# Performance work log

Measured on AMD Instinct MI355X. Metric: run time of the kernel, lower is better.

The kernel has to match this reference:

```python
import jax, jax.numpy as jnp
import numpy as np

D = 512
MOMENTUM = 0.99
NEG_INF = -1.0e9


def setup_inputs() -> dict:
    key = jax.random.key(0)
    ks = jax.random.split(key, 16)
    B, Lq, Lk = 16, 1024, 1024
    s = 0.02
    inp = {
        "uncond_q": jax.random.normal(ks[0], (B, D), jnp.float32),
        "q": jax.random.normal(ks[1], (B, Lq, D), jnp.float32),
        "k": jax.random.normal(ks[2], (B, Lk, D), jnp.float32),
        "v": jax.random.normal(ks[3], (B, Lk, D), jnp.float32),
        "src_key_padding_mask": jax.random.randint(ks[4], (B, Lk), 0, 2) > 0,
        "fallback_score": jnp.zeros((1,), jnp.float32),
        # parameters (torch Linear: y = x @ W.T + b)
        "Wv": jax.random.normal(ks[5], (D, D), jnp.float32) * s,
        "bv": jnp.zeros((D,), jnp.float32),
        "Wf": jax.random.normal(ks[6], (D, D), jnp.float32) * s,
        "bf": jnp.zeros((D,), jnp.float32),
        "W1": jax.random.normal(ks[7], (D, D), jnp.float32) * s,
        "b1": jnp.zeros((D,), jnp.float32),
        "W2": jax.random.normal(ks[8], (D // 2, D), jnp.float32) * s,
        "b2": jnp.zeros((D // 2,), jnp.float32),
        "W3": jax.random.normal(ks[9], (1, D // 2), jnp.float32) * s,
        "b3": jnp.zeros((1,), jnp.float32),
    }
    return inp


def _scorer(x, W1, b1, W2, b2, W3, b3):
    h = jax.nn.relu(x @ W1.T + b1)
    h = jax.nn.relu(h @ W2.T + b2)
    return jnp.tanh(h @ W3.T + b3)


def reference(uncond_q, q, k, v, src_key_padding_mask, fallback_score,
              Wv, bv, Wf, bf, W1, b1, W2, b2, W3, b3):
    B, Lq, _ = q.shape
    v_p = v @ Wv.T + bv                                  # [B,Lk,D]
    default_values = (uncond_q @ Wf.T + bf)[:, None, :]  # [B,1,D]

    scores = jnp.einsum('bqd,bkd->bqk', q, k) / jnp.sqrt(jnp.float32(D))

    # EMA fallback-score update (training mode), detached from grads
    bmax = jax.lax.stop_gradient(scores.max())
    bmin = jax.lax.stop_gradient(scores.min())
    fb = MOMENTUM * fallback_score[0] + (1.0 - MOMENTUM) * (bmax + bmin) / 2.0

    scores = jnp.where(src_key_padding_mask[:, None, :], NEG_INF, scores)
    fb_col = jnp.broadcast_to(fb, (B, Lq, 1))
    scores = jnp.concatenate([scores, fb_col], axis=-1)   # [B,Lq,Lk+1]
    weights = jax.nn.softmax(scores, axis=-1)

    v_padded = jnp.concatenate([v_p, default_values], axis=1)  # [B,Lk+1,D]
    out = jnp.einsum('bqk,bkd->bqd', weights, v_padded)

    return (_scorer(out, W1, b1, W2, b2, W3, b3),
            _scorer(default_values, W1, b1, W2, b2, W3, b3))
```

## Files before the change

### kernel.cpp

```cpp
#include <hip/hip_runtime.h>

typedef _Float16 f16;
typedef f16  f16x8 __attribute__((ext_vector_type(8)));
typedef f16  f16x4 __attribute__((ext_vector_type(4)));
typedef __fp16 fp16x2 __attribute__((ext_vector_type(2)));
typedef float f32x4 __attribute__((ext_vector_type(4)));

__device__ __forceinline__ void gld_lds16(const f16* g, void* l) {
  __builtin_amdgcn_global_load_lds((const __attribute__((address_space(1))) void*)g,
                                   (__attribute__((address_space(3))) void*)l,
                                   16, 0, 0);
}

__device__ __forceinline__ f16x8 pack8(float4 a, float4 b) {
  union { f16x8 v; fp16x2 h[4]; } u;
  u.h[0] = __builtin_amdgcn_cvt_pkrtz(a.x, a.y);
  u.h[1] = __builtin_amdgcn_cvt_pkrtz(a.z, a.w);
  u.h[2] = __builtin_amdgcn_cvt_pkrtz(b.x, b.y);
  u.h[3] = __builtin_amdgcn_cvt_pkrtz(b.z, b.w);
  return u.v;
}

enum { EPI_SCORES = 0, EPI_RELU = 2, EPI_OUT = 3, EPI_BIASR = 4 };

template<int EPI, bool XMAP>
__global__ __launch_bounds__(256)
void gemm_bt(const f16* __restrict__ A, const f16* __restrict__ B, void* __restrict__ C,
             int lda, int ldb, int ldc, int K,
             long long sA, long long sB, long long sC,
             const float* __restrict__ bias, float scale,
             const float* __restrict__ wfb, const float* __restrict__ dvv,
             int nx, int nbz)
{
  __shared__ __align__(16) f16 As[4][128][32];
  __shared__ __align__(16) f16 Bs[4][128][32];
  const int tid  = threadIdx.x;
  const int lane = tid & 63;
  const int w    = tid >> 6;
  const int wm   = w >> 1, wn = w & 1;

  const int lin = blockIdx.x;
  int bz, bj;
  if constexpr (XMAP) {
    const int xcd = lin & 7, rest = lin >> 3;
    const int grp = rest / nbz;
    bj = rest - grp * nbz;
    bz = xcd + (grp << 3);
  } else {
    bz = lin / nbz; bj = lin - bz * nbz;
  }
  const int m0 = (bj / nx) * 128, n0 = (bj % nx) * 128;
  const f16* Ab = A + (size_t)bz * sA + (size_t)m0 * lda;
  const f16* Bb = B + (size_t)bz * sB + (size_t)n0 * ldb;

  f32x4 acc[4][4] = {};
  const int nsteps = K >> 5;

#define STAGE(bufb, ks)                                                              \
  {                                                                                  \
    const int k0_ = (ks) << 5;                                                       \
    _Pragma("unroll")                                                                \
    for (int i = 0; i < 2; ++i) {                                                    \
      const int ci = i * 256 + tid;                                                  \
      const int r  = ci >> 2;                                                        \
      const int sg = (ci & 3) ^ ((r >> 1) & 3);                                      \
      gld_lds16(Ab + (size_t)r * lda + k0_ + sg * 8,                                 \
                (char*)As + (bufb) + (size_t)(i * 256 + w * 64) * 16);               \
      gld_lds16(Bb + (size_t)r * ldb + k0_ + sg * 8,                                 \
                (char*)Bs + (bufb) + (size_t)(i * 256 + w * 64) * 16);               \
    }                                                                                \
  }

  STAGE(0, 0)
  if (1 < nsteps) STAGE(8192, 1)
  if (2 < nsteps) STAGE(16384, 2)

  const int elemoff = (((lane >> 4) ^ ((lane >> 1) & 3)) << 3);

  int cur = 0;
  for (int t = 0; t < nsteps; ++t) {
    if (t + 2 < nsteps)      asm volatile("s_waitcnt vmcnt(8)" ::: "memory");
    else if (t + 1 < nsteps) asm volatile("s_waitcnt vmcnt(4)" ::: "memory");
    else                     asm volatile("s_waitcnt vmcnt(0)" ::: "memory");
    __builtin_amdgcn_s_barrier();
    __builtin_amdgcn_sched_barrier(0);
    if (t + 3 < nsteps) STAGE(((cur + 3) & 3) * 8192, t + 3)
    f16x8 af[4], bfr[4];
#pragma unroll
    for (int m = 0; m < 4; ++m)
      af[m] = *(const f16x8*)&As[cur][wm * 64 + m * 16 + (lane & 15)][elemoff];
#pragma unroll
    for (int n = 0; n < 4; ++n)
      bfr[n] = *(const f16x8*)&Bs[cur][wn * 64 + n * 16 + (lane & 15)][elemoff];
    __builtin_amdgcn_s_setprio(1);
#pragma unroll
    for (int m = 0; m < 4; ++m)
#pragma unroll
      for (int n = 0; n < 4; ++n)
        acc[m][n] = __builtin_amdgcn_mfma_f32_16x16x32_f16(af[m], bfr[n], acc[m][n], 0, 0, 0);
    __builtin_amdgcn_s_setprio(0);
    cur = (cur + 1) & 3;
  }
#undef STAGE

  const int col_l = lane & 15;
  const int row_l = (lane >> 4) << 2;

  {
    f16* Ch = (f16*)C + (size_t)bz * sC + (size_t)m0 * ldc + n0;
#pragma unroll
    for (int m = 0; m < 4; ++m)
#pragma unroll
      for (int n = 0; n < 4; ++n)
#pragma unroll
        for (int r = 0; r < 4; ++r) {
          const int rr = wm * 64 + m * 16 + row_l + r;
          const int cc = wn * 64 + n * 16 + col_l;
          float val = acc[m][n][r];
          if constexpr (EPI == EPI_RELU) { val += bias[n0 + cc]; val = fmaxf(val, 0.0f); }
          if constexpr (EPI == EPI_BIASR) val += bias[m0 + rr];
          if constexpr (EPI == EPI_OUT)
            val += wfb[bz * 1024 + m0 + rr] * dvv[bz * 512 + n0 + cc];
          Ch[(size_t)rr * ldc + cc] = (f16)val;
        }
  }
  (void)scale;
}

__global__ __launch_bounds__(512, 2)
void gemm256_scores(const float* __restrict__ A, const float* __restrict__ B, f16* __restrict__ C,
                    float scale, float* __restrict__ mmarr)
{
  __shared__ __align__(16) f16 As[3][256][32];
  __shared__ __align__(16) f16 Bs[3][256][32];
  __shared__ float redm[8], redn[8];
  const int tid  = threadIdx.x;
  const int lane = tid & 63;
  const int w    = tid >> 6;
  const int wm   = w >> 2, wn = w & 3;
  const int lin  = blockIdx.x;
  const int xcd = lin & 7, rest = lin >> 3;
  const int bj  = rest & 15;
  const int bz  = xcd + ((rest >> 4) << 3);
  const int m0 = (bj >> 2) * 256, n0 = (bj & 3) * 256;
  const float* Ab = A + (size_t)bz * 524288 + (size_t)m0 * 512;
  const float* Bb = B + (size_t)bz * 524288 + (size_t)n0 * 512;

  const int r0  = tid >> 2;
  const int sg0 = (tid & 3) ^ ((r0 >> 1) & 3);
  const size_t offG = (size_t)r0 * 512 + sg0 * 8;
  f16* const dstA0 = (f16*)As + (size_t)tid * 8;
  f16* const dstB0 = (f16*)Bs + (size_t)tid * 8;

  f32x4 acc[8][4] = {};

#pragma unroll
  for (int s = 0; s < 2; ++s) {
    const int k0 = s << 5;
    float4 a0 = *(const float4*)(Ab + offG + k0);
    float4 a1 = *(const float4*)(Ab + offG + k0 + 4);
    float4 a2 = *(const float4*)(Ab + offG + k0 + 65536);
    float4 a3 = *(const float4*)(Ab + offG + k0 + 65540);
    float4 b0 = *(const float4*)(Bb + offG + k0);
    float4 b1 = *(const float4*)(Bb + offG + k0 + 4);
    float4 b2 = *(const float4*)(Bb + offG + k0 + 65536);
    float4 b3 = *(const float4*)(Bb + offG + k0 + 65540);
    *(f16x8*)(dstA0 + s * 8192)        = pack8(a0, a1);
    *(f16x8*)(dstA0 + s * 8192 + 4096) = pack8(a2, a3);
    *(f16x8*)(dstB0 + s * 8192)        = pack8(b0, b1);
    *(f16x8*)(dstB0 + s * 8192 + 4096) = pack8(b2, b3);
  }
  __syncthreads();

  const int fr = lane & 15;
  const int elemoff = (((lane >> 4) ^ ((lane >> 1) & 3)) << 3);

  int cur = 0;
  for (int t = 0; t < 16; ++t) {
    float4 a0, a1, a2, a3, b0, b1, b2, b3;
    if (t + 2 < 16) {
      const int k0 = (t + 2) << 5;
      a0 = *(const float4*)(Ab + offG + k0);
      a1 = *(const float4*)(Ab + offG + k0 + 4);
      a2 = *(const float4*)(Ab + offG + k0 + 65536);
      a3 = *(const float4*)(Ab + offG + k0 + 65540);
      b0 = *(const float4*)(Bb + offG + k0);
      b1 = *(const float4*)(Bb + offG + k0 + 4);
      b2 = *(const float4*)(Bb + offG + k0 + 65536);
      b3 = *(const float4*)(Bb + offG + k0 + 65540);
    }
    f16x8 af[8], bfr[4];
#pragma unroll
    for (int m = 0; m < 8; ++m)
      af[m] = *(const f16x8*)&As[cur][wm * 128 + m * 16 + fr][elemoff];
#pragma unroll
    for (int n = 0; n < 4; ++n)
      bfr[n] = *(const f16x8*)&Bs[cur][wn * 64 + n * 16 + fr][elemoff];
    __builtin_amdgcn_s_setprio(1);
#pragma unroll
    for (int m = 0; m < 8; ++m)
#pragma unroll
      for (int n = 0; n < 4; ++n)
        acc[m][n] = __builtin_amdgcn_mfma_f32_16x16x32_f16(af[m], bfr[n], acc[m][n], 0, 0, 0);
    __builtin_amdgcn_s_setprio(0);
    if (t + 2 < 16) {
      int wb = cur + 2; if (wb >= 3) wb -= 3;
      *(f16x8*)(dstA0 + wb * 8192)        = pack8(a0, a1);
      *(f16x8*)(dstA0 + wb * 8192 + 4096) = pack8(a2, a3);
      *(f16x8*)(dstB0 + wb * 8192)        = pack8(b0, b1);
      *(f16x8*)(dstB0 + wb * 8192 + 4096) = pack8(b2, b3);
    }
    __syncthreads();
    cur = (cur + 1 == 3) ? 0 : cur + 1;
  }

  const int col_l = lane & 15;
  const int row_l = (lane >> 4) << 2;
  f16* Ch = C + (size_t)bz * 1048576 + (size_t)m0 * 1024 + n0;
  float lmax = -3.402823466e38f, lmin = 3.402823466e38f;
#pragma unroll
  for (int m = 0; m < 8; ++m)
#pragma unroll
    for (int n = 0; n < 4; ++n)
#pragma unroll
      for (int r = 0; r < 4; ++r) {
        float val = acc[m][n][r] * scale;
        lmax = fmaxf(lmax, val); lmin = fminf(lmin, val);
        Ch[(size_t)(wm * 128 + m * 16 + row_l + r) * 1024 + (wn * 64 + n * 16 + col_l)] = (f16)val;
      }
#pragma unroll
  for (int off = 32; off >= 1; off >>= 1) {
    lmax = fmaxf(lmax, __shfl_xor(lmax, off));
    lmin = fminf(lmin, __shfl_xor(lmin, off));
  }
  if (lane == 0) { redm[w] = lmax; redn[w] = lmin; }
  __syncthreads();
  if (tid == 0) {
    float gm = redm[0], gn = redn[0];
#pragma unroll
    for (int i = 1; i < 8; ++i) { gm = fmaxf(gm, redm[i]); gn = fminf(gn, redn[i]); }
    mmarr[lin] = gm; mmarr[256 + lin] = gn;
  }
}

__global__ __launch_bounds__(256)
void gemm_vpt(const f16* __restrict__ A, const float* __restrict__ B, f16* __restrict__ C,
              const float* __restrict__ bias)
{
  __shared__ __align__(16) f16 As[3][128][32];
  __shared__ __align__(16) f16 Bs[3][128][32];
  const int tid  = threadIdx.x;
  const int lane = tid & 63;
  const int w    = tid >> 6;
  const int wm   = w >> 1, wn = w & 1;
  const int lin  = blockIdx.x;
  const int xcd = lin & 7, rest = lin >> 3;
  const int grp = rest >> 5, bj = rest & 31;
  const int bz  = xcd + (grp << 3);
  const int m0 = (bj >> 3) * 128, n0 = (bj & 7) * 128;
  const f16*   Ab = A + (size_t)m0 * 512;
  const float* Bb = B + (size_t)bz * 524288 + (size_t)n0 * 512;

  const int r0  = tid >> 2;
  const int sg0 = (tid & 3) ^ ((r0 >> 1) & 3);
  const size_t offA = (size_t)r0 * 512 + sg0 * 8;
  const size_t offB = (size_t)r0 * 512 + sg0 * 8;
  f16* const dstA0 = (f16*)As + (size_t)tid * 8;
  f16* const dstB0 = (f16*)Bs + (size_t)tid * 8;

  f32x4 acc[4][4] = {};

#pragma unroll
  for (int s = 0; s < 2; ++s) {
    const int k0 = s << 5;
    f16x8  a0 = *(const f16x8*)(Ab + offA + k0);
    f16x8  a1 = *(const f16x8*)(Ab + offA + k0 + 32768);
    float4 b0 = *(const float4*)(Bb + offB + k0);
    float4 b1 = *(const float4*)(Bb + offB + k0 + 4);
    float4 b2 = *(const float4*)(Bb + offB + k0 + 32768);
    float4 b3 = *(const float4*)(Bb + offB + k0 + 32772);
    *(f16x8*)(dstA0 + s * 4096)        = a0;
    *(f16x8*)(dstA0 + s * 4096 + 2048) = a1;
    *(f16x8*)(dstB0 + s * 4096)        = pack8(b0, b1);
    *(f16x8*)(dstB0 + s * 4096 + 2048) = pack8(b2, b3);
  }
  __syncthreads();

  const int fr = lane & 15;
  const int elemoff = (((lane >> 4) ^ ((lane >> 1) & 3)) << 3);

  int cur = 0;
  for (int t = 0; t < 16; ++t) {
    f16x8  a0, a1; float4 b0, b1, b2, b3;
    if (t + 2 < 16) {
      const int k0 = (t + 2) << 5;
      a0 = *(const f16x8*)(Ab + offA + k0);
      a1 = *(const f16x8*)(Ab + offA + k0 + 32768);
      b0 = *(const float4*)(Bb + offB + k0);
      b1 = *(const float4*)(Bb + offB + k0 + 4);
      b2 = *(const float4*)(Bb + offB + k0 + 32768);
      b3 = *(const float4*)(Bb + offB + k0 + 32772);
    }
    f16x8 af[4], bfr[4];
#pragma unroll
    for (int m = 0; m < 4; ++m)
      af[m] = *(const f16x8*)&As[cur][wm * 64 + m * 16 + fr][elemoff];
#pragma unroll
    for (int n = 0; n < 4; ++n)
      bfr[n] = *(const f16x8*)&Bs[cur][wn * 64 + n * 16 + fr][elemoff];
    __builtin_amdgcn_s_setprio(1);
#pragma unroll
    for (int m = 0; m < 4; ++m)
#pragma unroll
      for (int n = 0; n < 4; ++n)
        acc[m][n] = __builtin_amdgcn_mfma_f32_16x16x32_f16(af[m], bfr[n], acc[m][n], 0, 0, 0);
    __builtin_amdgcn_s_setprio(0);
    if (t + 2 < 16) {
      int wb = cur + 2; if (wb >= 3) wb -= 3;
      *(f16x8*)(dstA0 + wb * 4096)        = a0;
      *(f16x8*)(dstA0 + wb * 4096 + 2048) = a1;
      *(f16x8*)(dstB0 + wb * 4096)        = pack8(b0, b1);
      *(f16x8*)(dstB0 + wb * 4096 + 2048) = pack8(b2, b3);
    }
    __syncthreads();
    cur = (cur + 1 == 3) ? 0 : cur + 1;
  }

  const int col_l = lane & 15;
  const int row_l = (lane >> 4) << 2;
  f16* Ch = C + (size_t)bz * 524288 + (size_t)m0 * 1024 + n0;
#pragma unroll
  for (int m = 0; m < 4; ++m)
#pragma unroll
    for (int n = 0; n < 4; ++n)
#pragma unroll
      for (int r = 0; r < 4; ++r) {
        const int rr = wm * 64 + m * 16 + row_l + r;
        const int cc = wn * 64 + n * 16 + col_l;
        Ch[(size_t)rr * 1024 + cc] = (f16)(acc[m][n][r] + bias[m0 + rr]);
      }
}

__global__ __launch_bounds__(256)
void front_k(const float* __restrict__ wv, const float* __restrict__ w1,
             const float* __restrict__ w2,
             f16* __restrict__ owv, f16* __restrict__ ow1, f16* __restrict__ ow2,
             const float* __restrict__ uq, const float* __restrict__ Wf,
             const float* __restrict__ bfv, float* __restrict__ dv,
             const unsigned char* __restrict__ mask, unsigned* __restrict__ mm)
{
  const int blk = blockIdx.x;
  if (blk < 640) {
    int i = blk * 256 + threadIdx.x;
    const float* src; f16* dst; int j;
    if (i < 65536)       { src = wv; dst = owv; j = i; }
    else if (i < 131072) { src = w1; dst = ow1; j = i - 65536; }
    else                 { src = w2; dst = ow2; j = i - 131072; }
    float4 x = *(const float4*)(src + (size_t)j * 4);
    f16x4 o = { (f16)x.x, (f16)x.y, (f16)x.z, (f16)x.w };
    *(f16x4*)(dst + (size_t)j * 4) = o;
  } else if (blk < 2688) {
    const int gw   = ((blk - 640) * 256 + threadIdx.x) >> 6;
    const int lane = threadIdx.x & 63;
    const int b = gw >> 9, j = gw & 511;
    const float* x  = uq + (size_t)b * 512;
    const float* wr = Wf + (size_t)j * 512;
    const int o = lane * 8;
    float4 x0 = *(const float4*)(x + o),  x1 = *(const float4*)(x + o + 4);
    float4 w0 = *(const float4*)(wr + o), w1v = *(const float4*)(wr + o + 4);
    float s = x0.x*w0.x + x0.y*w0.y + x0.z*w0.z + x0.w*w0.w
            + x1.x*w1v.x + x1.y*w1v.y + x1.z*w1v.z + x1.w*w1v.w;
#pragma unroll
    for (int off = 32; off >= 1; off >>= 1) s += __shfl_xor(s, off);
    if (lane == 0) dv[gw] = s + bfv[j];
  } else {
    __shared__ int redc[256];
    int c = 0;
    for (int i = threadIdx.x; i < 16384; i += 256) c += (mask[i] != 0) ? 1 : 0;
    redc[threadIdx.x] = c;
    __syncthreads();
    for (int s = 128; s > 0; s >>= 1) {
      if (threadIdx.x < s) redc[threadIdx.x] += redc[threadIdx.x + s];
      __syncthreads();
    }
    if (threadIdx.x == 0) mm[0] = (unsigned)redc[0];
  }
}

__global__ __launch_bounds__(256)
void softmax_rows(const f16* __restrict__ scores, const void* __restrict__ maskp,
                  const float* __restrict__ fallback, const float* __restrict__ mmarr,
                  const unsigned* __restrict__ mm,
                  f16* __restrict__ Wt, float* __restrict__ wfb)
{
  __shared__ float red[8];
  const int row  = blockIdx.x;
  const int b    = row >> 10;
  const int tid  = threadIdx.x;
  const int lane = tid & 63, w = tid >> 6;

  float mx0 = mmarr[tid];
  float mn0 = mmarr[256 + tid];
#pragma unroll
  for (int off = 32; off >= 1; off >>= 1) {
    mx0 = fmaxf(mx0, __shfl_xor(mx0, off));
    mn0 = fminf(mn0, __shfl_xor(mn0, off));
  }
  if (lane == 0) { red[w] = mx0; red[4 + w] = mn0; }
  __syncthreads();
  const float gmax = fmaxf(fmaxf(red[0], red[1]), fmaxf(red[2], red[3]));
  const float gmin = fminf(fminf(red[4], red[5]), fminf(red[6], red[7]));
  const float fb = 0.99f * fallback[0] + 0.005f * (gmax + gmin);
  const unsigned mode = (mm[0] > 5000u) ? 1u : 0u;
  __syncthreads();

  const f16* s = scores + (size_t)row * 1024;
  const int k0 = tid * 4;
  f16x4 sv = *(const f16x4*)(s + k0);
  float x[4];
  if (mode) {
    const unsigned char* m8 = (const unsigned char*)maskp + b * 1024 + k0;
    x[0] = m8[0] ? -1e9f : (float)sv[0];  x[1] = m8[1] ? -1e9f : (float)sv[1];
    x[2] = m8[2] ? -1e9f : (float)sv[2];  x[3] = m8[3] ? -1e9f : (float)sv[3];
  } else {
    const int* mi = (const int*)maskp + b * 1024 + k0;
    x[0] = mi[0] ? -1e9f : (float)sv[0];  x[1] = mi[1] ? -1e9f : (float)sv[1];
    x[2] = mi[2] ? -1e9f : (float)sv[2];  x[3] = mi[3] ? -1e9f : (float)sv[3];
  }
  float mx = fmaxf(fmaxf(x[0], x[1]), fmaxf(x[2], x[3]));
#pragma unroll
  for (int off = 32; off >= 1; off >>= 1) mx = fmaxf(mx, __shfl_xor(mx, off));
  if (lane == 0) red[w] = mx;
  __syncthreads();
  mx = fmaxf(fmaxf(fmaxf(red[0], red[1]), fmaxf(red[2], red[3])), fb);
  float e0 = expf(x[0] - mx), e1 = expf(x[1] - mx), e2 = expf(x[2] - mx), e3 = expf(x[3] - mx);
  float sum = (e0 + e1) + (e2 + e3);
#pragma unroll
  for (int off = 32; off >= 1; off >>= 1) sum += __shfl_xor(sum, off);
  if (lane == 0) red[4 + w] = sum;
  __syncthreads();
  float efb = expf(fb - mx);
  float Z = ((red[4] + red[5]) + (red[6] + red[7])) + efb;
  float inv = 1.0f / Z;
  f16x4 o = { (f16)(e0 * inv), (f16)(e1 * inv), (f16)(e2 * inv), (f16)(e3 * inv) };
  *(f16x4*)&Wt[(size_t)row * 1024 + k0] = o;
  if (tid == 0) wfb[row] = efb * inv;
}

template<int IN, int ACT>
__global__ __launch_bounds__(256)
void fc_wave(const float* __restrict__ X, const float* __restrict__ W,
             const float* __restrict__ bias, float* __restrict__ Y, int OutN)
{
  const int gw   = (blockIdx.x * 256 + threadIdx.x) >> 6;
  const int lane = threadIdx.x & 63;
  const int b = gw / OutN, j = gw - b * OutN;
  const float* x  = X + (size_t)b * IN;
  const float* wr = W + (size_t)j * IN;
  float s = 0.f;
  if constexpr (IN == 512) {
    const int o = lane * 8;
    float4 x0 = *(const float4*)(x + o),  x1 = *(const float4*)(x + o + 4);
    float4 w0 = *(const float4*)(wr + o), w1 = *(const float4*)(wr + o + 4);
    s = x0.x*w0.x + x0.y*w0.y + x0.z*w0.z + x0.w*w0.w
      + x1.x*w1.x + x1.y*w1.y + x1.z*w1.z + x1.w*w1.w;
  } else {
    const int o = lane * 4;
    float4 x0 = *(const float4*)(x + o);
    float4 w0 = *(const float4*)(wr + o);
    s = x0.x*w0.x + x0.y*w0.y + x0.z*w0.z + x0.w*w0.w;
  }
#pragma unroll
  for (int off = 32; off >= 1; off >>= 1) s += __shfl_xor(s, off);
  if (lane == 0) {
    float val = s + bias[ACT == 2 ? 0 : j];
    if constexpr (ACT == 1) val = fmaxf(val, 0.f);
    if constexpr (ACT == 2) val = tanhf(val);
    Y[gw] = val;
  }
}

__global__ __launch_bounds__(256)
void y_kernel(const f16* __restrict__ h2, const float* __restrict__ W3,
              const float* __restrict__ b3, float* __restrict__ outp)
{
  int row = blockIdx.x * 16 + (threadIdx.x >> 4);
  int l   = threadIdx.x & 15;
  const f16* h = h2 + (size_t)row * 256 + l * 16;
  float s = 0.f;
#pragma unroll
  for (int j = 0; j < 16; ++j) s += (float)h[j] * W3[l * 16 + j];
#pragma unroll
  for (int off = 1; off < 16; off <<= 1) s += __shfl_xor(s, off);
  if (l == 0) outp[row] = tanhf(s + b3[0]);
}

extern "C" void kernel_launch(void* const* d_in, const int* in_sizes, int n_in,
                              void* d_out, int out_size, void* d_ws, size_t ws_size,
                              hipStream_t stream) {
  const float* uq       = (const float*)d_in[0];
  const float* q        = (const float*)d_in[1];
  const float* kk       = (const float*)d_in[2];
  const float* v        = (const float*)d_in[3];
  const void*  mask     = d_in[4];
  const float* fallback = (const float*)d_in[5];
  const float* Wv = (const float*)d_in[6];
  const float* bv = (const float*)d_in[7];
  const float* Wf = (const float*)d_in[8];
  const float* bf = (const float*)d_in[9];
  const float* W1 = (const float*)d_in[10];
  const float* b1 = (const float*)d_in[11];
  const float* W2 = (const float*)d_in[12];
  const float* b2 = (const float*)d_in[13];
  const float* W3 = (const float*)d_in[14];
  const float* b3 = (const float*)d_in[15];
  float* outp = (float*)d_out;

  char* ws = (char*)d_ws;
  const size_t MB = 1ull << 20;
  f16*  scores = (f16*)ws;
  f16*  h1b  = (f16*)ws;
  f16*  h2b  = (f16*)(ws + 16 * MB);
  f16*  vpt  = (f16*)(ws + 32 * MB);
  f16*  outb = (f16*)(ws + 48 * MB);
  f16*  wts  = (f16*)(ws + 64 * MB);
  char* cst  = ws + 112 * MB;
  f16*  Wv16 = (f16*)(cst);
  f16*  W116 = (f16*)(cst + 512 * 1024);
  f16*  W216 = (f16*)(cst + 1024 * 1024);
  float* dv   = (float*)(cst + 1280 * 1024);
  float* wfb  = (float*)(cst + 1312 * 1024);
  float* h1d  = (float*)(cst + 1376 * 1024);
  float* h2d  = (float*)(cst + 1408 * 1024);
  unsigned* mm = (unsigned*)(cst + 1424 * 1024);
  float* mmarr = (float*)(cst + 1432 * 1024);

  front_k<<<2689, 256, 0, stream>>>(Wv, W1, W2, Wv16, W116, W216,
                                    uq, Wf, bf, dv,
                                    (const unsigned char*)mask, mm);

  gemm256_scores<<<256, 512, 0, stream>>>(q, kk, scores, 0.04419417382415922f, mmarr);

  softmax_rows<<<16384, 256, 0, stream>>>(scores, mask, fallback, mmarr, mm, wts, wfb);

  gemm_vpt<<<512, 256, 0, stream>>>(Wv16, v, vpt, bv);

  gemm_bt<EPI_OUT, true><<<512, 256, 0, stream>>>(
      wts, vpt, outb, 1024, 1024, 512, 1024,
      1048576LL, 524288LL, 524288LL,
      nullptr, 1.f, wfb, dv, 4, 32);

  gemm_bt<EPI_RELU, false><<<512, 256, 0, stream>>>(
      outb, W116, h1b, 512, 512, 512, 512, 0LL, 0LL, 0LL,
      b1, 1.f, nullptr, nullptr, 4, 512);

  gemm_bt<EPI_RELU, false><<<256, 256, 0, stream>>>(
      h1b, W216, h2b, 512, 512, 256, 512, 0LL, 0LL, 0LL,
      b2, 1.f, nullptr, nullptr, 2, 256);

  y_kernel<<<1024, 256, 0, stream>>>(h2b, W3, b3, outp);

  fc_wave<512, 1><<<2048, 256, 0, stream>>>(dv, W1, b1, h1d, 512);
  fc_wave<512, 1><<<1024, 256, 0, stream>>>(h1d, W2, b2, h2d, 256);
  fc_wave<256, 2><<<4, 256, 0, stream>>>(h2d, W3, b3, outp + 16384, 1);

  (void)in_sizes; (void)n_in; (void)out_size; (void)ws_size;
}
```

Baseline: 161.3 us.

## Hold global prefetch in registers one stage ahead and relax loop barrier

The fp32-to-fp16 scores GEMM loop now loads the tile for step t+3 into registers and writes the registers loaded in the previous iteration into the LDS ring before the MFMAs. Previously each tile was loaded and stored to LDS within the same iteration. Global load latency now gets a full iteration to resolve. The full __syncthreads is replaced by an lgkmcnt wait plus a raw s_barrier, so outstanding global loads are not drained at each barrier. This raises register pressure through the held prefetch values and depends on the manual waitcnt being correct.

```diff
diff --git a/kernel.cpp b/kernel.cpp
--- a/kernel.cpp
+++ b/kernel.cpp
@@ -170,6 +170,18 @@
     *(f16x8*)(dstB0 + s * 8192)        = pack8(b0, b1);
     *(f16x8*)(dstB0 + s * 8192 + 4096) = pack8(b2, b3);
   }
+  float4 ha0, ha1, ha2, ha3, hb0, hb1, hb2, hb3;
+  {
+    const int k0 = 2 << 5;
+    ha0 = *(const float4*)(Ab + offG + k0);
+    ha1 = *(const float4*)(Ab + offG + k0 + 4);
+    ha2 = *(const float4*)(Ab + offG + k0 + 65536);
+    ha3 = *(const float4*)(Ab + offG + k0 + 65540);
+    hb0 = *(const float4*)(Bb + offG + k0);
+    hb1 = *(const float4*)(Bb + offG + k0 + 4);
+    hb2 = *(const float4*)(Bb + offG + k0 + 65536);
+    hb3 = *(const float4*)(Bb + offG + k0 + 65540);
+  }
   __syncthreads();
 
   const int fr = lane & 15;
@@ -177,18 +189,6 @@
 
   int cur = 0;
   for (int t = 0; t < 16; ++t) {
-    float4 a0, a1, a2, a3, b0, b1, b2, b3;
-    if (t + 2 < 16) {
-      const int k0 = (t + 2) << 5;
-      a0 = *(const float4*)(Ab + offG + k0);
-      a1 = *(const float4*)(Ab + offG + k0 + 4);
-      a2 = *(const float4*)(Ab + offG + k0 + 65536);
-      a3 = *(const float4*)(Ab + offG + k0 + 65540);
-      b0 = *(const float4*)(Bb + offG + k0);
-      b1 = *(const float4*)(Bb + offG + k0 + 4);
-      b2 = *(const float4*)(Bb + offG + k0 + 65536);
-      b3 = *(const float4*)(Bb + offG + k0 + 65540);
-    }
     f16x8 af[8], bfr[4];
 #pragma unroll
     for (int m = 0; m < 8; ++m)
@@ -196,6 +196,24 @@
 #pragma unroll
     for (int n = 0; n < 4; ++n)
       bfr[n] = *(const f16x8*)&Bs[cur][wn * 64 + n * 16 + fr][elemoff];
+    if (t + 2 < 16) {
+      int wb = cur + 2; if (wb >= 3) wb -= 3;
+      *(f16x8*)(dstA0 + wb * 8192)        = pack8(ha0, ha1);
+      *(f16x8*)(dstA0 + wb * 8192 + 4096) = pack8(ha2, ha3);
+      *(f16x8*)(dstB0 + wb * 8192)        = pack8(hb0, hb1);
+      *(f16x8*)(dstB0 + wb * 8192 + 4096) = pack8(hb2, hb3);
+    }
+    if (t + 3 < 16) {
+      const int k0 = (t + 3) << 5;
+      ha0 = *(const float4*)(Ab + offG + k0);
+      ha1 = *(const float4*)(Ab + offG + k0 + 4);
+      ha2 = *(const float4*)(Ab + offG + k0 + 65536);
+      ha3 = *(const float4*)(Ab + offG + k0 + 65540);
+      hb0 = *(const float4*)(Bb + offG + k0);
+      hb1 = *(const float4*)(Bb + offG + k0 + 4);
+      hb2 = *(const float4*)(Bb + offG + k0 + 65536);
+      hb3 = *(const float4*)(Bb + offG + k0 + 65540);
+    }
     __builtin_amdgcn_s_setprio(1);
 #pragma unroll
     for (int m = 0; m < 8; ++m)
@@ -203,14 +221,9 @@
       for (int n = 0; n < 4; ++n)
         acc[m][n] = __builtin_amdgcn_mfma_f32_16x16x32_f16(af[m], bfr[n], acc[m][n], 0, 0, 0);
     __builtin_amdgcn_s_setprio(0);
-    if (t + 2 < 16) {
-      int wb = cur + 2; if (wb >= 3) wb -= 3;
-      *(f16x8*)(dstA0 + wb * 8192)        = pack8(a0, a1);
-      *(f16x8*)(dstA0 + wb * 8192 + 4096) = pack8(a2, a3);
-      *(f16x8*)(dstB0 + wb * 8192)        = pack8(b0, b1);
-      *(f16x8*)(dstB0 + wb * 8192 + 4096) = pack8(b2, b3);
-    }
-    __syncthreads();
+    asm volatile("s_waitcnt lgkmcnt(0)" ::: "memory");
+    __builtin_amdgcn_sched_barrier(0);
+    __builtin_amdgcn_s_barrier();
     cur = (cur + 1 == 3) ? 0 : cur + 1;
   }
 
```

Result: no change. 160.8 us, median of 2 (-0.4%).
